# Kernel tuning notes

Measured on AMD Instinct MI355X. Metric: run time of the kernel, lower is better.

## Reference

```python
import jax, jax.numpy as jnp
import numpy as np

B, L, D = 4, 2048, 1024   # batch, seq_len, input_channels
S = 4096                  # param_token_num
DV = 1024                 # output_channels


def setup_inputs() -> dict:
    key = jax.random.key(0)
    k1, k2, k3 = jax.random.split(key, 3)
    return {
        "inputs": jax.random.normal(k1, (B, L, D), dtype=jnp.float32),
        "key_param_tokens": jax.random.normal(k2, (S, D), dtype=jnp.float32),
        "value_param_tokens": jax.random.normal(k3, (S, DV), dtype=jnp.float32),
    }


def reference(inputs, key_param_tokens, value_param_tokens):
    # scores: [B, L, S] — full score matrix (this is what a fused kernel would avoid)
    scores = jnp.einsum("bld,sd->bls", inputs, key_param_tokens)
    # gelu_l2_norm: exact (erf) gelu, then L2-normalize over S and rescale by sqrt(S)
    g = jax.nn.gelu(scores, approximate=False)
    l2 = jnp.linalg.norm(g, axis=-1, keepdims=True)
    w = g / l2 * jnp.sqrt(jnp.asarray(g.shape[-1], g.dtype))
    # weighted sum over param value tokens: [B, L, DV]
    return jnp.einsum("bls,sv->blv", w, value_param_tokens)
```

## Files before the change

kernel.cpp:

```cpp
#include <hip/hip_runtime.h>
#include <hip/hip_bf16.h>
#include <stdint.h>

#define M_ROWS 8192
#define D_DIM  1024
#define S_DIM  4096
#define DV_DIM 1024

typedef __attribute__((ext_vector_type(8))) short bf16x8;
typedef __attribute__((ext_vector_type(4))) float f32x4;
typedef unsigned short u16;

static __device__ __forceinline__ u16 f2bf(float x) {
  union { float f; unsigned u; } v; v.f = x;
  unsigned r = v.u + 0x7FFFu + ((v.u >> 16) & 1u);
  return (u16)(r >> 16);
}
static __device__ __forceinline__ float bf2f(u16 h) {
  union { unsigned u; float f; } v; v.u = ((unsigned)h) << 16;
  return v.f;
}
static __device__ __forceinline__ float gelu_fast(float x) {
  float u = 0.7978845608028654f * x * (1.0f + 0.044715f * x * x);
  float e = __expf(2.0f * u);
  float t = 1.0f - 2.0f / (e + 1.0f);
  return 0.5f * x * (1.0f + t);
}

static __device__ __forceinline__ void gload16(const void* g, void* l) {
  __builtin_amdgcn_global_load_lds(
      (__attribute__((address_space(1))) void*)(void*)(g),
      (__attribute__((address_space(3))) void*)(l), 16, 0, 0);
}

__global__ __launch_bounds__(256)
void cast_f32_bf16(const float* __restrict__ in, u16* __restrict__ out, int n4) {
  const int i = blockIdx.x * 256 + threadIdx.x;
  if (i >= n4) return;
  const float4 v = ((const float4*)in)[i];
  ushort4 o;
  o.x = f2bf(v.x); o.y = f2bf(v.y); o.z = f2bf(v.z); o.w = f2bf(v.w);
  ((ushort4*)out)[i] = o;
}

__global__ __launch_bounds__(256)
void transpose_cast(const float* __restrict__ V, u16* __restrict__ VT, int R, int C) {
  __shared__ float tile[32][33];
  const int tx = threadIdx.x & 31;
  const int ty = threadIdx.x >> 5;
  const int r0 = blockIdx.y * 32;
  const int c0 = blockIdx.x * 32;
#pragma unroll
  for (int dy = 0; dy < 32; dy += 8)
    tile[ty + dy][tx] = V[(long)(r0 + ty + dy) * C + (c0 + tx)];
  __syncthreads();
#pragma unroll
  for (int dy = 0; dy < 32; dy += 8)
    VT[(long)(c0 + ty + dy) * R + (r0 + tx)] = f2bf(tile[tx][ty + dy]);
}

__global__ __launch_bounds__(256)
void row_scale(const u16* __restrict__ G, float* __restrict__ scale, int S) {
  const int row = blockIdx.x;
  const u16* g = G + (long)row * S;
  float ssq = 0.f;
  for (int i = threadIdx.x * 8; i < S; i += 256 * 8) {
    bf16x8 v = *(const bf16x8*)&g[i];
#pragma unroll
    for (int j = 0; j < 8; ++j) {
      float f = bf2f((u16)v[j]);
      ssq += f * f;
    }
  }
#pragma unroll
  for (int off = 32; off > 0; off >>= 1)
    ssq += __shfl_down(ssq, off, 64);
  __shared__ float wsum[4];
  if ((threadIdx.x & 63) == 0) wsum[threadIdx.x >> 6] = ssq;
  __syncthreads();
  if (threadIdx.x == 0) {
    float t = wsum[0] + wsum[1] + wsum[2] + wsum[3];
    scale[row] = 64.0f * rsqrtf(t + 1e-30f);
  }
}


#define VM4 asm volatile("s_waitcnt vmcnt(4)" ::: "memory")
#define VM2 asm volatile("s_waitcnt vmcnt(2)" ::: "memory")
#define VM0 asm volatile("s_waitcnt vmcnt(0)" ::: "memory")

#define PHASE(P, STAGES, WAITS)                                               \
  {                                                                           \
    bf16x8 af[2][2];                                                          \
    _Pragma("unroll")                                                         \
    for (int j = 0; j < 2; ++j) {                                             \
      const int ar = wm * 128 + ((P) * 2 + j) * 16 + fr;                      \
      af[j][0] = rdfrag(la, ar, 0);                                           \
      af[j][1] = rdfrag(la, ar, 1);                                           \
    }                                                                         \
    STAGES;                                                                   \
    __builtin_amdgcn_s_barrier();                                             \
    asm volatile("s_waitcnt lgkmcnt(0)" ::: "memory");                        \
    __builtin_amdgcn_sched_barrier(0);                                        \
    __builtin_amdgcn_s_setprio(1);                                            \
    _Pragma("unroll")                                                         \
    for (int j = 0; j < 2; ++j) {                                             \
      _Pragma("unroll")                                                       \
      for (int n = 0; n < NF; ++n) {                                          \
        acc[(P) * 2 + j][n] = __builtin_amdgcn_mfma_f32_16x16x32_bf16(        \
            af[j][0], bfr[n][0], acc[(P) * 2 + j][n], 0, 0, 0);               \
        acc[(P) * 2 + j][n] = __builtin_amdgcn_mfma_f32_16x16x32_bf16(        \
            af[j][1], bfr[n][1], acc[(P) * 2 + j][n], 0, 0, 0);               \
      }                                                                       \
    }                                                                         \
    __builtin_amdgcn_s_setprio(0);                                            \
    WAITS;                                                                    \
    __builtin_amdgcn_s_barrier();                                             \
  }

#define READ_B                                                                \
  {                                                                           \
    _Pragma("unroll")                                                         \
    for (int n = 0; n < NF; ++n) {                                            \
      const int br = wn * WNT + n * 16 + fr;                                  \
      bfr[n][0] = rdfrag(lb, br, 0);                                          \
      bfr[n][1] = rdfrag(lb, br, 1);                                          \
    }                                                                         \
  }

template <int MODE, int BN>
__global__ __launch_bounds__(512, 2)
void gemm8p(const u16* __restrict__ A, const u16* __restrict__ Bm,
            void* __restrict__ Cout, const float* __restrict__ scale,
            const int K, const int N, const int nBN, const int nWG) {
  constexpr int BM = 256, BK = 64;
  constexpr int WNT = BN / 4;
  constexpr int NF = WNT / 16;

  __shared__ u16 ldsA[2][BM * BK];
  __shared__ u16 ldsB[2][BN * BK];

  const int tid = threadIdx.x;
  const int lane = tid & 63;
  const int wv = tid >> 6;
  const int wm = wv >> 2, wn = wv & 3;
  const int fr = lane & 15, hi = lane >> 4;

  int wg;
  {
    const int q = nWG >> 3, r = nWG & 7;
    const int x = blockIdx.x & 7, ix = blockIdx.x >> 3;
    wg = (x < r ? x * (q + 1) : r * (q + 1) + (x - r) * q) + ix;
  }
  const int bm = wg / nBN, bn = wg % nBN;
  const long aR0 = (long)bm * BM;
  const long bR0 = (long)bn * BN;

  const int srow = tid >> 3;
  const int sch = (tid & 7) ^ (srow & 7);
  const long aoff = (aR0 + srow) * (long)K + sch * 8;
  const long boff = (bR0 + srow) * (long)K + sch * 8;

  auto SA = [&](int buf, int r, int kOff) {
    gload16(A + aoff + ((long)r * 64) * K + kOff, &ldsA[buf][r * 4096 + tid * 8]);
  };
  auto SB = [&](int buf, int r, int kOff) {
    gload16(Bm + boff + ((long)r * 64) * K + kOff, &ldsB[buf][r * 4096 + tid * 8]);
  };
  auto rdfrag = [&](const u16* base, int row, int kk) -> bf16x8 {
    return *(const bf16x8*)&base[row * 64 + (((kk << 2) | hi) ^ (row & 7)) * 8];
  };

  f32x4 acc[8][NF];
#pragma unroll
  for (int m = 0; m < 8; ++m)
#pragma unroll
    for (int n = 0; n < NF; ++n)
      acc[m][n] = f32x4{0.f, 0.f, 0.f, 0.f};

  bf16x8 bfr[NF][2];
  const int nK = K / BK;

  if constexpr (BN == 256) {
    SB(0, 0, 0); SB(0, 1, 0); SB(0, 2, 0); SB(0, 3, 0);
  } else {
    SB(0, 0, 0); SB(0, 1, 0);
  }
  SA(0, 0, 0); SA(0, 2, 0); SA(0, 1, 0); SA(0, 3, 0);
  VM2;
  __builtin_amdgcn_s_barrier();

  int cur = 0;
  for (int kt = 0; kt < nK - 1; ++kt) {
    const int kN = (kt + 1) * BK;
    const int nxt = cur ^ 1;
    const u16* la = ldsA[cur];
    const u16* lb = ldsB[cur];
    READ_B;
    if constexpr (BN == 256) {
      PHASE(0, { SB(nxt, 0, kN); SB(nxt, 1, kN); }, {});
      PHASE(1, { SB(nxt, 2, kN); SB(nxt, 3, kN); }, VM4);
      PHASE(2, { SA(nxt, 0, kN); SA(nxt, 2, kN); }, {});
      PHASE(3, { SA(nxt, 1, kN); SA(nxt, 3, kN); }, VM2);
    } else {
      PHASE(0, { SB(nxt, 0, kN); SB(nxt, 1, kN); }, {});
      PHASE(1, { SA(nxt, 0, kN); SA(nxt, 2, kN); }, VM4);
      PHASE(2, { SA(nxt, 1, kN); SA(nxt, 3, kN); }, {});
      PHASE(3, {}, VM2);
    }
    cur ^= 1;
  }

  {
    const u16* la = ldsA[cur];
    const u16* lb = ldsB[cur];
    READ_B;
    PHASE(0, {}, {});
    PHASE(1, {}, VM0);
    PHASE(2, {}, {});
    PHASE(3, {}, {});
  }

  const long row0 = aR0 + wm * 128;
  const long col0 = bR0 + wn * WNT;
  if constexpr (MODE == 0) {
    u16* Cg = (u16*)Cout;
#pragma unroll
    for (int m = 0; m < 8; ++m) {
#pragma unroll
      for (int i = 0; i < 4; ++i) {
        const long r = row0 + m * 16 + hi * 4 + i;
#pragma unroll
        for (int n = 0; n < NF; ++n)
          Cg[r * N + col0 + n * 16 + fr] = f2bf(gelu_fast(acc[m][n][i]));
      }
    }
  } else {
    float* Cf = (float*)Cout;
#pragma unroll
    for (int m = 0; m < 8; ++m) {
#pragma unroll
      for (int i = 0; i < 4; ++i) {
        const long r = row0 + m * 16 + hi * 4 + i;
        const float s = scale[r];
#pragma unroll
        for (int n = 0; n < NF; ++n)
          Cf[r * N + col0 + n * 16 + fr] = acc[m][n][i] * s;
      }
    }
  }
}

extern "C" void kernel_launch(void* const* d_in, const int* in_sizes, int n_in,
                              void* d_out, int out_size, void* d_ws, size_t ws_size,
                              hipStream_t stream) {
  const float* Qf = (const float*)d_in[0];
  const float* Kf = (const float*)d_in[1];
  const float* Vf = (const float*)d_in[2];
  float* Out = (float*)d_out;

  const int M = M_ROWS, D = D_DIM, S = S_DIM, DV = DV_DIM;

  char* p = (char*)d_ws;
  u16* Qb = (u16*)p;            p += (size_t)M * D * 2;
  u16* Kb = (u16*)p;            p += (size_t)S * D * 2;
  u16* VT = (u16*)p;            p += (size_t)DV * S * 2;
  float* scalebuf = (float*)p;  p += (size_t)M * 4;
  u16* G = (u16*)p;
  const size_t fixed = (size_t)(p - (char*)d_ws);
  const size_t avail = (ws_size > fixed) ? (ws_size - fixed) : 0;

  const size_t bytes_per_row = (size_t)S * 2;
  size_t rows_fit = avail / bytes_per_row;
  int chunk = (int)((rows_fit / 256) * 256);
  if (chunk > M) chunk = M;
  if (chunk < 256) chunk = 256;

  cast_f32_bf16<<<(M * D / 4 + 255) / 256, 256, 0, stream>>>(Qf, Qb, M * D / 4);
  cast_f32_bf16<<<(S * D / 4 + 255) / 256, 256, 0, stream>>>(Kf, Kb, S * D / 4);
  transpose_cast<<<dim3(DV / 32, S / 32), 256, 0, stream>>>(Vf, VT, S, DV);

  const int nBN1 = S / 256;
  const int nBN2 = DV / 128;
  for (int m0 = 0; m0 < M; m0 += chunk) {
    const int rows = (M - m0 < chunk) ? (M - m0) : chunk;
    const int nWG1 = (rows / 256) * nBN1;
    gemm8p<0, 256><<<dim3(nWG1), 512, 0, stream>>>(
        Qb + (size_t)m0 * D, Kb, (void*)G, nullptr, D, S, nBN1, nWG1);
    row_scale<<<rows, 256, 0, stream>>>(G, scalebuf, S);
    const int nWG2 = (rows / 256) * nBN2;
    gemm8p<1, 128><<<dim3(nWG2), 512, 0, stream>>>(
        G, VT, (void*)(Out + (size_t)m0 * DV), scalebuf, S, DV, nBN2, nWG2);
  }
}
```

Before: 197.5 us.

## Fuse row L2-norm computation into second GEMM's A-fragment reads

Removes the separate row_scale kernel. The second GEMM now accumulates the sum of squares of G from the A fragments it already loads, with the work split across the four wn waves by k-tile. The sums are reduced across waves through LDS at the epilogue and turned into per-row scales there. The PHASE barrier also drops the explicit lgkmcnt(0) wait and sched_barrier, which may change instruction scheduling and risks LDS-read hazards. The extra ALU work in the MFMA loop costs a little, in exchange for skipping one pass over G in global memory plus a kernel launch.

```diff
diff --git a/kernel.cpp b/kernel.cpp
--- a/kernel.cpp
+++ b/kernel.cpp
@@ -59,32 +59,8 @@
     VT[(long)(c0 + ty + dy) * R + (r0 + tx)] = f2bf(tile[tx][ty + dy]);
 }
 
-__global__ __launch_bounds__(256)
-void row_scale(const u16* __restrict__ G, float* __restrict__ scale, int S) {
-  const int row = blockIdx.x;
-  const u16* g = G + (long)row * S;
-  float ssq = 0.f;
-  for (int i = threadIdx.x * 8; i < S; i += 256 * 8) {
-    bf16x8 v = *(const bf16x8*)&g[i];
-#pragma unroll
-    for (int j = 0; j < 8; ++j) {
-      float f = bf2f((u16)v[j]);
-      ssq += f * f;
-    }
-  }
-#pragma unroll
-  for (int off = 32; off > 0; off >>= 1)
-    ssq += __shfl_down(ssq, off, 64);
-  __shared__ float wsum[4];
-  if ((threadIdx.x & 63) == 0) wsum[threadIdx.x >> 6] = ssq;
-  __syncthreads();
-  if (threadIdx.x == 0) {
-    float t = wsum[0] + wsum[1] + wsum[2] + wsum[3];
-    scale[row] = 64.0f * rsqrtf(t + 1e-30f);
-  }
-}
-
-
+
+#define BARRIER asm volatile("s_barrier" ::: "memory")
 #define VM4 asm volatile("s_waitcnt vmcnt(4)" ::: "memory")
 #define VM2 asm volatile("s_waitcnt vmcnt(2)" ::: "memory")
 #define VM0 asm volatile("s_waitcnt vmcnt(0)" ::: "memory")
@@ -99,9 +75,7 @@
       af[j][1] = rdfrag(la, ar, 1);                                           \
     }                                                                         \
     STAGES;                                                                   \
-    __builtin_amdgcn_s_barrier();                                             \
-    asm volatile("s_waitcnt lgkmcnt(0)" ::: "memory");                        \
-    __builtin_amdgcn_sched_barrier(0);                                        \
+    BARRIER;                                                                  \
     __builtin_amdgcn_s_setprio(1);                                            \
     _Pragma("unroll")                                                         \
     for (int j = 0; j < 2; ++j) {                                             \
@@ -114,8 +88,23 @@
       }                                                                       \
     }                                                                         \
     __builtin_amdgcn_s_setprio(0);                                            \
+    if constexpr (MODE == 1) {                                                \
+      if (((kt) & 3) == wn) {                                                 \
+        _Pragma("unroll")                                                     \
+        for (int j = 0; j < 2; ++j) {                                         \
+          _Pragma("unroll")                                                   \
+          for (int q = 0; q < 2; ++q) {                                       \
+            _Pragma("unroll")                                                 \
+            for (int e = 0; e < 8; ++e) {                                     \
+              const float f_ = bf2f((u16)af[j][q][e]);                        \
+              sqacc[(P) * 2 + j] += f_ * f_;                                  \
+            }                                                                 \
+          }                                                                   \
+        }                                                                     \
+      }                                                                       \
+    }                                                                         \
     WAITS;                                                                    \
-    __builtin_amdgcn_s_barrier();                                             \
+    BARRIER;                                                                  \
   }
 
 #define READ_B                                                                \
@@ -131,8 +120,9 @@
 template <int MODE, int BN>
 __global__ __launch_bounds__(512, 2)
 void gemm8p(const u16* __restrict__ A, const u16* __restrict__ Bm,
-            void* __restrict__ Cout, const float* __restrict__ scale,
-            const int K, const int N, const int nBN, const int nWG) {
+            void* __restrict__ Cout,
+            const int K, const int lda, const int ldb,
+            const int N, const int nBN, const int nWG) {
   constexpr int BM = 256, BK = 64;
   constexpr int WNT = BN / 4;
   constexpr int NF = WNT / 16;
@@ -158,14 +148,14 @@
 
   const int srow = tid >> 3;
   const int sch = (tid & 7) ^ (srow & 7);
-  const long aoff = (aR0 + srow) * (long)K + sch * 8;
-  const long boff = (bR0 + srow) * (long)K + sch * 8;
+  const long aoff = (aR0 + srow) * (long)lda + sch * 8;
+  const long boff = (bR0 + srow) * (long)ldb + sch * 8;
 
   auto SA = [&](int buf, int r, int kOff) {
-    gload16(A + aoff + ((long)r * 64) * K + kOff, &ldsA[buf][r * 4096 + tid * 8]);
+    gload16(A + aoff + ((long)r * 64) * lda + kOff, &ldsA[buf][r * 4096 + tid * 8]);
   };
   auto SB = [&](int buf, int r, int kOff) {
-    gload16(Bm + boff + ((long)r * 64) * K + kOff, &ldsB[buf][r * 4096 + tid * 8]);
+    gload16(Bm + boff + ((long)r * 64) * ldb + kOff, &ldsB[buf][r * 4096 + tid * 8]);
   };
   auto rdfrag = [&](const u16* base, int row, int kk) -> bf16x8 {
     return *(const bf16x8*)&base[row * 64 + (((kk << 2) | hi) ^ (row & 7)) * 8];
@@ -178,6 +168,8 @@
     for (int n = 0; n < NF; ++n)
       acc[m][n] = f32x4{0.f, 0.f, 0.f, 0.f};
 
+  float sqacc[8] = {0.f, 0.f, 0.f, 0.f, 0.f, 0.f, 0.f, 0.f};
+
   bf16x8 bfr[NF][2];
   const int nK = K / BK;
 
@@ -188,7 +180,7 @@
   }
   SA(0, 0, 0); SA(0, 2, 0); SA(0, 1, 0); SA(0, 3, 0);
   VM2;
-  __builtin_amdgcn_s_barrier();
+  BARRIER;
 
   int cur = 0;
   for (int kt = 0; kt < nK - 1; ++kt) {
@@ -212,6 +204,8 @@
   }
 
   {
+    const int kt = nK - 1;
+    (void)kt;
     const u16* la = ldsA[cur];
     const u16* lb = ldsB[cur];
     READ_B;
@@ -236,13 +230,29 @@
       }
     }
   } else {
+    float* red = (float*)&ldsA[0][0];
+#pragma unroll
+    for (int m = 0; m < 8; ++m) {
+      float s = sqacc[m];
+      s += __shfl_xor(s, 16);
+      s += __shfl_xor(s, 32);
+      if (hi == 0) red[(wm * 128 + m * 16 + fr) * 4 + wn] = s;
+    }
+    BARRIER;
+    float* scl = (float*)&ldsB[0][0];
+    if (tid < 256) {
+      const float4 v = *(const float4*)&red[tid * 4];
+      scl[tid] = 64.0f * rsqrtf(v.x + v.y + v.z + v.w + 1e-30f);
+    }
+    BARRIER;
     float* Cf = (float*)Cout;
 #pragma unroll
     for (int m = 0; m < 8; ++m) {
 #pragma unroll
       for (int i = 0; i < 4; ++i) {
-        const long r = row0 + m * 16 + hi * 4 + i;
-        const float s = scale[r];
+        const int rl = wm * 128 + m * 16 + hi * 4 + i;
+        const long r = aR0 + rl;
+        const float s = scl[rl];
 #pragma unroll
         for (int n = 0; n < NF; ++n)
           Cf[r * N + col0 + n * 16 + fr] = acc[m][n][i] * s;
@@ -265,7 +275,6 @@
   u16* Qb = (u16*)p;            p += (size_t)M * D * 2;
   u16* Kb = (u16*)p;            p += (size_t)S * D * 2;
   u16* VT = (u16*)p;            p += (size_t)DV * S * 2;
-  float* scalebuf = (float*)p;  p += (size_t)M * 4;
   u16* G = (u16*)p;
   const size_t fixed = (size_t)(p - (char*)d_ws);
   const size_t avail = (ws_size > fixed) ? (ws_size - fixed) : 0;
@@ -286,10 +295,9 @@
     const int rows = (M - m0 < chunk) ? (M - m0) : chunk;
     const int nWG1 = (rows / 256) * nBN1;
     gemm8p<0, 256><<<dim3(nWG1), 512, 0, stream>>>(
-        Qb + (size_t)m0 * D, Kb, (void*)G, nullptr, D, S, nBN1, nWG1);
-    row_scale<<<rows, 256, 0, stream>>>(G, scalebuf, S);
+        Qb + (size_t)m0 * D, Kb, (void*)G, D, D, D, S, nBN1, nWG1);
     const int nWG2 = (rows / 256) * nBN2;
     gemm8p<1, 128><<<dim3(nWG2), 512, 0, stream>>>(
-        G, VT, (void*)(Out + (size_t)m0 * DV), scalebuf, S, DV, nBN2, nWG2);
-  }
-}
+        G, VT, (void*)(Out + (size_t)m0 * DV), S, S, S, DV, nBN2, nWG2);
+  }
+}
```

After: 219.6 us. +11.2%, slower.
